# Kernel tuning notes

Hardware: AMD Instinct MI355X
Metric: run time of the kernel (lower is better)

The kernel has to match this reference:

```python
import jax, jax.numpy as jnp
import numpy as np
from jax import lax

K_RATIO = 0.5  # args['k_ratio'], eval (non-training) branch
K_SIZE = 5     # args['gaussian_smooth']['k_size']
C_SIGMA = 1.0  # args['gaussian_smooth']['c_sigma']


def _gaussian_kernel(k_size=K_SIZE, sigma=C_SIGMA):
    # matches Communication.init_gaussian_filter (note: 2*pi*sigma, not sigma^2, as in source)
    c = k_size // 2
    x, y = np.mgrid[-c:k_size - c, -c:k_size - c]
    g = 1.0 / (2.0 * np.pi * sigma) * np.exp(-(np.square(x) + np.square(y)) / (2.0 * np.square(sigma)))
    return jnp.asarray(g, jnp.float32)[None, None]  # (1,1,k,k) OIHW, bias is zero


def setup_inputs() -> dict:
    key = jax.random.key(0)
    conf = jax.random.normal(jax.random.fold_in(key, 1), (8, 6, 4, 512, 512), jnp.float32)
    warp = jnp.ones((8, 1, 512, 512), jnp.float32)
    return {"confidence_maps": conf, "warp_masks": warp, "gauss_kernel": _gaussian_kernel()}


def reference(confidence_maps, warp_masks, gauss_kernel):
    # confidence_maps: (B, L, C, H, W); warp_masks: (B, 1, H, W); gauss_kernel: (1,1,k,k)
    B, L, C, H, W = confidence_maps.shape
    # sigmoid + max over anchor dim, keepdim -> (B, L, 1, H, W)
    m = jnp.max(jax.nn.sigmoid(confidence_maps), axis=2, keepdims=True)
    m = m * warp_masks[:, None]  # broadcast warp mask over agents
    # frozen gaussian smoothing conv, SAME padding (stride 1, pad (k-1)//2)
    sm = lax.conv_general_dilated(m.reshape(B * L, 1, H, W), gauss_kernel,
                                  window_strides=(1, 1), padding='SAME',
                                  dimension_numbers=('NCHW', 'OIHW', 'NCHW'))
    flat = sm.reshape(B, L, H * W)
    K = int(H * W * K_RATIO)  # static k, eval k_ratio branch
    _, idx = lax.top_k(flat, K)  # (B, L, K)
    mask = jnp.zeros_like(flat).at[
        jnp.arange(B)[:, None, None], jnp.arange(L)[None, :, None], idx
    ].set(1.0)  # scatter ones at top-k positions
    # communication rate computed BEFORE ego mask is forced to 1 (as in source)
    rate = jnp.mean(jnp.sum(mask[:, 1:], axis=(1, 2)) / ((L - 1) * H * W))
    mask = mask.reshape(B, L, H, W).at[:, 0].set(1.0)  # ego agent keeps everything
    return mask.reshape(B * L, 1, H, W), rate
```

## Files before the change

kernel.cpp:

```cpp
#include <hip/hip_runtime.h>


#define NROWSEL 40
#define NPIX    262144
#define KSEL    131072
#define CAND_CAP 512
#define KAPPA    3
#define KSCALE   1048576.0f
#define KMAX     1048575.0f

#define OFF_KEY  0ull
#define OFF_H1   41943040ull
#define OFF_H2   42106880ull
#define OFF_ST   42270720ull
#define OFF_CC   42271040ull
#define OFF_CI   42271200ull
#define OFF_CK   42353120ull
#define META_U32 82040

__device__ __forceinline__ float m_val_f32(const float* __restrict__ confr,
                                           const float* __restrict__ warpr,
                                           int gy, int gx) {
  if (gy < 0 || gy >= 512 || gx < 0 || gx >= 512) return 0.0f;
  int off = gy * 512 + gx;
  float x0 = confr[off];
  float x1 = confr[NPIX + off];
  float x2 = confr[2 * NPIX + off];
  float x3 = confr[3 * NPIX + off];
  float mx = fmaxf(fmaxf(x0, x1), fmaxf(x2, x3));
  float s = 1.0f / (1.0f + expf(-mx));
  return s * warpr[off];
}

__device__ __forceinline__ double m_val(const float* __restrict__ confr,
                                        const float* __restrict__ warpr,
                                        int gy, int gx) {
  if (gy < 0 || gy >= 512 || gx < 0 || gx >= 512) return 0.0;
  int off = gy * 512 + gx;
  float x0 = confr[off];
  float x1 = confr[NPIX + off];
  float x2 = confr[2 * NPIX + off];
  float x3 = confr[3 * NPIX + off];
  float mx = fmaxf(fmaxf(x0, x1), fmaxf(x2, x3));
  double s = 1.0 / (1.0 + exp(-(double)mx));
  return s * (double)warpr[off];
}

__device__ __forceinline__ void scan1024(const unsigned* __restrict__ hs,
                                         unsigned* __restrict__ red,
                                         int tid, unsigned cum0,
                                         int* bsel, unsigned* above) {
  red[tid] = hs[tid * 4] + hs[tid * 4 + 1] + hs[tid * 4 + 2] + hs[tid * 4 + 3];
  __syncthreads();
  if (tid == 0) {
    unsigned cum = cum0;
    *bsel = 0; *above = cum0;
    for (int c = 255; c >= 0; --c) {
      if (cum + red[c] >= (unsigned)KSEL) {
        unsigned cc2 = cum;
        for (int k = 3; k >= 0; --k) {
          unsigned hv = hs[c * 4 + k];
          if (cc2 + hv >= (unsigned)KSEL) { *bsel = c * 4 + k; *above = cc2; break; }
          cc2 += hv;
        }
        break;
      }
      cum += red[c];
    }
  }
}

__global__ void ego_fill_kernel(float* __restrict__ out,
                                unsigned* __restrict__ meta) {
  int i = blockIdx.x * 256 + threadIdx.x;
  int b = i >> 16;
  int o4 = i & 65535;
  float4* p = (float4*)(out + (size_t)b * 6u * NPIX) + o4;
  *p = make_float4(1.f, 1.f, 1.f, 1.f);
  if (i < META_U32) meta[i] = 0u;
}

__global__ __launch_bounds__(256) void compute_kernel(
    const float* __restrict__ conf, const float* __restrict__ warp,
    const float* __restrict__ gk, unsigned* __restrict__ keys,
    unsigned* __restrict__ hist1) {
  const int blk = blockIdx.x;
  const int j = blk >> 6;
  const int tile = blk & 63;
  const int ty0 = (tile >> 3) << 6;
  const int tx0 = (tile & 7) << 6;
  const int b = j / 5;
  const int l = j % 5 + 1;
  const int rowg = b * 6 + l;
  const float* confr = conf + (size_t)rowg * 4u * NPIX;
  const float* warpr = warp + (size_t)b * NPIX;

  __shared__ float mt[68][68];
  __shared__ float ht[68][64];
  __shared__ unsigned lh[4096];
  __shared__ float wr[5], wc[5];
  const int tid = threadIdx.x;
  if (tid < 5) {
    wr[tid] = gk[10 + tid];
    wc[tid] = gk[tid * 5 + 2] / gk[12];
  }
  for (int i = tid; i < 4096; i += 256) lh[i] = 0u;

  for (int i = tid; i < 68 * 68; i += 256) {
    int hy = i / 68, hx = i - hy * 68;
    mt[hy][hx] = m_val_f32(confr, warpr, ty0 + hy - 2, tx0 + hx - 2);
  }
  __syncthreads();

  for (int i = tid; i < 68 * 64; i += 256) {
    int hy = i >> 6, x = i & 63;
    float a = mt[hy][x] * wr[0];
    a = fmaf(wr[1], mt[hy][x + 1], a);
    a = fmaf(wr[2], mt[hy][x + 2], a);
    a = fmaf(wr[3], mt[hy][x + 3], a);
    a = fmaf(wr[4], mt[hy][x + 4], a);
    ht[hy][x] = a;
  }
  __syncthreads();

  const int txl = tid & 63;
  const int tyl = tid >> 6;
  const int cpy = tid & 3;
  unsigned* keyrow = keys + (size_t)j * NPIX;
  for (int rr = 0; rr < 16; ++rr) {
    int yy = tyl + (rr << 2);
    float acc = ht[yy][txl] * wc[0];
    acc = fmaf(wc[1], ht[yy + 1][txl], acc);
    acc = fmaf(wc[2], ht[yy + 2][txl], acc);
    acc = fmaf(wc[3], ht[yy + 3][txl], acc);
    acc = fmaf(wc[4], ht[yy + 4][txl], acc);
    unsigned k = (unsigned)fminf(fmaxf(acc * KSCALE, 0.0f), KMAX);
    keyrow[(ty0 + yy) * 512 + (tx0 + txl)] = k;
    atomicAdd(&lh[(k >> 10) * 4 + cpy], 1u);
  }
  __syncthreads();
  for (int i = tid; i < 1024; i += 256) {
    unsigned s = lh[i * 4] + lh[i * 4 + 1] + lh[i * 4 + 2] + lh[i * 4 + 3];
    if (s) atomicAdd(&hist1[j * 1024 + i], s);
  }
}

__global__ __launch_bounds__(256) void hist2_kernel(
    const unsigned* __restrict__ keys, const unsigned* __restrict__ hist1,
    unsigned* __restrict__ hist2) {
  int blk = blockIdx.x;
  int j = blk >> 5, seg = blk & 31;
  __shared__ unsigned hs[1024];
  __shared__ unsigned red[256];
  __shared__ unsigned lh[4096];
  __shared__ int s_b1;
  int tid = threadIdx.x;
  for (int i = tid; i < 1024; i += 256) hs[i] = hist1[j * 1024 + i];
  for (int i = tid; i < 4096; i += 256) lh[i] = 0u;
  __syncthreads();
  int b1; unsigned A1;
  scan1024(hs, red, tid, 0u, &b1, &A1);
  if (tid == 0) s_b1 = b1;
  __syncthreads();
  unsigned ub1 = (unsigned)s_b1;
  const uint4* kp = (const uint4*)(keys + (size_t)j * NPIX + seg * 8192);
  int c = tid & 3;
#pragma unroll
  for (int it = 0; it < 8; ++it) {
    uint4 k4 = kp[tid + it * 256];
    if ((k4.x >> 10) == ub1) atomicAdd(&lh[(k4.x & 1023u) * 4 + c], 1u);
    if ((k4.y >> 10) == ub1) atomicAdd(&lh[(k4.y & 1023u) * 4 + c], 1u);
    if ((k4.z >> 10) == ub1) atomicAdd(&lh[(k4.z & 1023u) * 4 + c], 1u);
    if ((k4.w >> 10) == ub1) atomicAdd(&lh[(k4.w & 1023u) * 4 + c], 1u);
  }
  __syncthreads();
  for (int i = tid; i < 1024; i += 256) {
    unsigned s = lh[i * 4] + lh[i * 4 + 1] + lh[i * 4 + 2] + lh[i * 4 + 3];
    if (s) atomicAdd(&hist2[j * 1024 + i], s);
  }
}

__global__ __launch_bounds__(256) void mask_gather_kernel(
    const unsigned* __restrict__ keys, const unsigned* __restrict__ hist1,
    const unsigned* __restrict__ hist2, float* __restrict__ out,
    int* __restrict__ st, unsigned* __restrict__ ccount,
    int* __restrict__ cidx, unsigned* __restrict__ ckey) {
  int blk = blockIdx.x;
  int j = blk >> 5, seg = blk & 31;
  int b = j / 5, l = j % 5 + 1;
  int rowg = b * 6 + l;
  __shared__ unsigned hs[1024];
  __shared__ unsigned red[256];
  __shared__ int s_pstar;
  int tid = threadIdx.x;
  for (int i = tid; i < 1024; i += 256) hs[i] = hist1[j * 1024 + i];
  __syncthreads();
  int b1; unsigned A1;
  scan1024(hs, red, tid, 0u, &b1, &A1);
  __syncthreads();
  for (int i = tid; i < 1024; i += 256) hs[i] = hist2[j * 1024 + i];
  __syncthreads();
  int b2; unsigned A2;
  scan1024(hs, red, tid, (tid == 0) ? A1 : 0u, &b2, &A2);
  if (tid == 0) {
    s_pstar = (b1 << 10) | b2;
    if (seg == 0) { st[j * 2] = s_pstar; st[j * 2 + 1] = (int)A2; }
  }
  __syncthreads();
  int pstar = s_pstar;

  const uint4* kp = (const uint4*)(keys + (size_t)j * NPIX + seg * 8192);
  float4* o4 = (float4*)(out + (size_t)rowg * NPIX + seg * 8192);
#pragma unroll
  for (int it = 0; it < 8; ++it) {
    int q = tid + it * 256;
    uint4 k4 = kp[q];
    unsigned w[4] = {k4.x, k4.y, k4.z, k4.w};
    float4 mv;
    float* mf = (float*)&mv;
#pragma unroll
    for (int e = 0; e < 4; ++e) {
      int k = (int)w[e];
      mf[e] = k > pstar + KAPPA ? 1.f : 0.f;
      if (k >= pstar - KAPPA && k <= pstar + KAPPA) {
        unsigned s = atomicAdd(&ccount[j], 1u);
        if (s < CAND_CAP) {
          cidx[j * CAND_CAP + s] = seg * 8192 + q * 4 + e;
          ckey[j * CAND_CAP + s] = (unsigned)k;
        }
      }
    }
    o4[q] = mv;
  }
}

__global__ __launch_bounds__(256) void resolve_kernel(
    const float* __restrict__ conf, const float* __restrict__ warp,
    const float* __restrict__ gk, const int* __restrict__ st,
    const unsigned* __restrict__ ccount, const int* __restrict__ cidx,
    const unsigned* __restrict__ ckey, float* __restrict__ out) {
  int j = blockIdx.x;
  int b = j / 5, l = j % 5 + 1;
  int rowg = b * 6 + l;
  const float* confr = conf + (size_t)rowg * 4u * NPIX;
  const float* warpr = warp + (size_t)b * NPIX;
  __shared__ double vs[CAND_CAP];
  __shared__ int ids[CAND_CAP];
  __shared__ unsigned red[256];
  __shared__ double g[25];
  int tid = threadIdx.x;
  if (tid < 25) g[tid] = (double)gk[tid];
  int pstar = st[j * 2];
  int A2 = st[j * 2 + 1];
  int C = (int)min(ccount[j], (unsigned)CAND_CAP);
  __syncthreads();
  unsigned cnt = 0;
  for (int i = tid; i < C; i += 256) {
    int idx = cidx[j * CAND_CAP + i];
    cnt += (int)ckey[j * CAND_CAP + i] > pstar ? 1u : 0u;
    int y = idx >> 9, x = idx & 511;
    double acc = 0.0;
#pragma unroll
    for (int dy = 0; dy < 5; ++dy)
#pragma unroll
      for (int dx = 0; dx < 5; ++dx)
        acc = fma(g[dy * 5 + dx], m_val(confr, warpr, y + dy - 2, x + dx - 2), acc);
    vs[i] = acc;
    ids[i] = idx;
  }
  red[tid] = cnt;
  __syncthreads();
  for (int s = 128; s > 0; s >>= 1) {
    if (tid < s) red[tid] += red[tid + s];
    __syncthreads();
  }
  int R = KSEL - A2 + (int)red[0];
  for (int i = tid; i < C; i += 256) {
    double vi = vs[i];
    int ii = ids[i];
    int rank = 0;
    for (int q = 0; q < C; ++q) {
      double vq = vs[q];
      rank += (vq > vi) || (vq == vi && ids[q] < ii) ? 1 : 0;
    }
    if (rank < R) out[(size_t)rowg * NPIX + ii] = 1.0f;
  }
  if (j == 0 && tid == 0) out[12582912] = 0.5f;
}

extern "C" void kernel_launch(void* const* d_in, const int* in_sizes, int n_in,
                              void* d_out, int out_size, void* d_ws, size_t ws_size,
                              hipStream_t stream) {
  const float* conf = (const float*)d_in[0];
  const float* warp = (const float*)d_in[1];
  const float* gk   = (const float*)d_in[2];
  float* out = (float*)d_out;
  char* ws = (char*)d_ws;

  unsigned* keys = (unsigned*)(ws + OFF_KEY);
  unsigned* h1   = (unsigned*)(ws + OFF_H1);
  unsigned* h2   = (unsigned*)(ws + OFF_H2);
  int*      st   = (int*)(ws + OFF_ST);
  unsigned* cc   = (unsigned*)(ws + OFF_CC);
  int*      ci   = (int*)(ws + OFF_CI);
  unsigned* ck   = (unsigned*)(ws + OFF_CK);

  ego_fill_kernel<<<2048, 256, 0, stream>>>(out, h1);
  compute_kernel<<<NROWSEL * 64, 256, 0, stream>>>(conf, warp, gk, keys, h1);
  hist2_kernel<<<NROWSEL * 32, 256, 0, stream>>>(keys, h1, h2);
  mask_gather_kernel<<<NROWSEL * 32, 256, 0, stream>>>(keys, h1, h2, out, st, cc, ci, ck);
  resolve_kernel<<<NROWSEL, 256, 0, stream>>>(conf, warp, gk, st, cc, ci, ck, out);
}
```

Baseline: 149.7 us.

## Fuse separable blur passes in registers and rebalance radix histogram to 256/4096 bins

```diff
diff --git a/kernel.cpp b/kernel.cpp
--- a/kernel.cpp
+++ b/kernel.cpp
@@ -11,12 +11,12 @@
 
 #define OFF_KEY  0ull
 #define OFF_H1   41943040ull
-#define OFF_H2   42106880ull
-#define OFF_ST   42270720ull
-#define OFF_CC   42271040ull
-#define OFF_CI   42271200ull
-#define OFF_CK   42353120ull
-#define META_U32 82040
+#define OFF_H2   41984000ull
+#define OFF_ST   42639360ull
+#define OFF_CC   42639680ull
+#define OFF_CI   42639840ull
+#define OFF_CK   42721760ull
+#define META_U32 174200
 
 __device__ __forceinline__ float m_val_f32(const float* __restrict__ confr,
                                            const float* __restrict__ warpr,
@@ -46,11 +46,25 @@
   return s * (double)warpr[off];
 }
 
-__device__ __forceinline__ void scan1024(const unsigned* __restrict__ hs,
+__device__ __forceinline__ void scan256(const unsigned* __restrict__ cs,
+                                        unsigned cum0, int& bsel,
+                                        unsigned& above) {
+  unsigned cum = cum0;
+  bsel = 0; above = cum0;
+  for (int c = 255; c >= 0; --c) {
+    if (cum + cs[c] >= (unsigned)KSEL) { bsel = c; above = cum; break; }
+    cum += cs[c];
+  }
+}
+
+__device__ __forceinline__ void scan4096(const unsigned* __restrict__ hs,
                                          unsigned* __restrict__ red,
                                          int tid, unsigned cum0,
                                          int* bsel, unsigned* above) {
-  red[tid] = hs[tid * 4] + hs[tid * 4 + 1] + hs[tid * 4 + 2] + hs[tid * 4 + 3];
+  unsigned s = 0;
+#pragma unroll 4
+  for (int k = 0; k < 16; ++k) s += hs[tid * 16 + k];
+  red[tid] = s;
   __syncthreads();
   if (tid == 0) {
     unsigned cum = cum0;
@@ -58,9 +72,9 @@
     for (int c = 255; c >= 0; --c) {
       if (cum + red[c] >= (unsigned)KSEL) {
         unsigned cc2 = cum;
-        for (int k = 3; k >= 0; --k) {
-          unsigned hv = hs[c * 4 + k];
-          if (cc2 + hv >= (unsigned)KSEL) { *bsel = c * 4 + k; *above = cc2; break; }
+        for (int k = 15; k >= 0; --k) {
+          unsigned hv = hs[c * 16 + k];
+          if (cc2 + hv >= (unsigned)KSEL) { *bsel = c * 16 + k; *above = cc2; break; }
           cc2 += hv;
         }
         break;
@@ -96,15 +110,14 @@
   const float* warpr = warp + (size_t)b * NPIX;
 
   __shared__ float mt[68][68];
-  __shared__ float ht[68][64];
-  __shared__ unsigned lh[4096];
+  __shared__ unsigned lh[1024];
   __shared__ float wr[5], wc[5];
   const int tid = threadIdx.x;
   if (tid < 5) {
     wr[tid] = gk[10 + tid];
     wc[tid] = gk[tid * 5 + 2] / gk[12];
   }
-  for (int i = tid; i < 4096; i += 256) lh[i] = 0u;
+  for (int i = tid; i < 1024; i += 256) lh[i] = 0u;
 
   for (int i = tid; i < 68 * 68; i += 256) {
     int hy = i / 68, hx = i - hy * 68;
@@ -112,36 +125,38 @@
   }
   __syncthreads();
 
-  for (int i = tid; i < 68 * 64; i += 256) {
-    int hy = i >> 6, x = i & 63;
-    float a = mt[hy][x] * wr[0];
-    a = fmaf(wr[1], mt[hy][x + 1], a);
-    a = fmaf(wr[2], mt[hy][x + 2], a);
-    a = fmaf(wr[3], mt[hy][x + 3], a);
-    a = fmaf(wr[4], mt[hy][x + 4], a);
-    ht[hy][x] = a;
-  }
-  __syncthreads();
-
   const int txl = tid & 63;
-  const int tyl = tid >> 6;
+  const int y0 = (tid >> 6) << 4;
   const int cpy = tid & 3;
   unsigned* keyrow = keys + (size_t)j * NPIX;
-  for (int rr = 0; rr < 16; ++rr) {
-    int yy = tyl + (rr << 2);
-    float acc = ht[yy][txl] * wc[0];
-    acc = fmaf(wc[1], ht[yy + 1][txl], acc);
-    acc = fmaf(wc[2], ht[yy + 2][txl], acc);
-    acc = fmaf(wc[3], ht[yy + 3][txl], acc);
-    acc = fmaf(wc[4], ht[yy + 4][txl], acc);
+
+#define HROW(r) ({ float a_ = mt[(r)][txl] * wr[0];            \
+                   a_ = fmaf(wr[1], mt[(r)][txl + 1], a_);     \
+                   a_ = fmaf(wr[2], mt[(r)][txl + 2], a_);     \
+                   a_ = fmaf(wr[3], mt[(r)][txl + 3], a_);     \
+                   fmaf(wr[4], mt[(r)][txl + 4], a_); })
+
+  float h0 = HROW(y0);
+  float h1 = HROW(y0 + 1);
+  float h2 = HROW(y0 + 2);
+  float h3 = HROW(y0 + 3);
+  for (int yy = y0; yy < y0 + 16; ++yy) {
+    float h4 = HROW(yy + 4);
+    float acc = h0 * wc[0];
+    acc = fmaf(wc[1], h1, acc);
+    acc = fmaf(wc[2], h2, acc);
+    acc = fmaf(wc[3], h3, acc);
+    acc = fmaf(wc[4], h4, acc);
     unsigned k = (unsigned)fminf(fmaxf(acc * KSCALE, 0.0f), KMAX);
     keyrow[(ty0 + yy) * 512 + (tx0 + txl)] = k;
-    atomicAdd(&lh[(k >> 10) * 4 + cpy], 1u);
-  }
-  __syncthreads();
-  for (int i = tid; i < 1024; i += 256) {
-    unsigned s = lh[i * 4] + lh[i * 4 + 1] + lh[i * 4 + 2] + lh[i * 4 + 3];
-    if (s) atomicAdd(&hist1[j * 1024 + i], s);
+    atomicAdd(&lh[(k >> 12) * 4 + cpy], 1u);
+    h0 = h1; h1 = h2; h2 = h3; h3 = h4;
+  }
+#undef HROW
+  __syncthreads();
+  if (tid < 256) {
+    unsigned s = lh[tid * 4] + lh[tid * 4 + 1] + lh[tid * 4 + 2] + lh[tid * 4 + 3];
+    if (s) atomicAdd(&hist1[j * 256 + tid], s);
   }
 }
 
@@ -150,33 +165,34 @@
     unsigned* __restrict__ hist2) {
   int blk = blockIdx.x;
   int j = blk >> 5, seg = blk & 31;
-  __shared__ unsigned hs[1024];
-  __shared__ unsigned red[256];
-  __shared__ unsigned lh[4096];
+  __shared__ unsigned hs[256];
+  __shared__ unsigned lh[8192];
   __shared__ int s_b1;
   int tid = threadIdx.x;
-  for (int i = tid; i < 1024; i += 256) hs[i] = hist1[j * 1024 + i];
-  for (int i = tid; i < 4096; i += 256) lh[i] = 0u;
-  __syncthreads();
-  int b1; unsigned A1;
-  scan1024(hs, red, tid, 0u, &b1, &A1);
-  if (tid == 0) s_b1 = b1;
+  hs[tid] = hist1[j * 256 + tid];
+  for (int i = tid; i < 8192; i += 256) lh[i] = 0u;
+  __syncthreads();
+  if (tid == 0) {
+    int b1; unsigned A1;
+    scan256(hs, 0u, b1, A1);
+    s_b1 = b1;
+  }
   __syncthreads();
   unsigned ub1 = (unsigned)s_b1;
   const uint4* kp = (const uint4*)(keys + (size_t)j * NPIX + seg * 8192);
-  int c = tid & 3;
+  int c = tid & 1;
 #pragma unroll
   for (int it = 0; it < 8; ++it) {
     uint4 k4 = kp[tid + it * 256];
-    if ((k4.x >> 10) == ub1) atomicAdd(&lh[(k4.x & 1023u) * 4 + c], 1u);
-    if ((k4.y >> 10) == ub1) atomicAdd(&lh[(k4.y & 1023u) * 4 + c], 1u);
-    if ((k4.z >> 10) == ub1) atomicAdd(&lh[(k4.z & 1023u) * 4 + c], 1u);
-    if ((k4.w >> 10) == ub1) atomicAdd(&lh[(k4.w & 1023u) * 4 + c], 1u);
-  }
-  __syncthreads();
-  for (int i = tid; i < 1024; i += 256) {
-    unsigned s = lh[i * 4] + lh[i * 4 + 1] + lh[i * 4 + 2] + lh[i * 4 + 3];
-    if (s) atomicAdd(&hist2[j * 1024 + i], s);
+    if ((k4.x >> 12) == ub1) atomicAdd(&lh[(k4.x & 4095u) * 2 + c], 1u);
+    if ((k4.y >> 12) == ub1) atomicAdd(&lh[(k4.y & 4095u) * 2 + c], 1u);
+    if ((k4.z >> 12) == ub1) atomicAdd(&lh[(k4.z & 4095u) * 2 + c], 1u);
+    if ((k4.w >> 12) == ub1) atomicAdd(&lh[(k4.w & 4095u) * 2 + c], 1u);
+  }
+  __syncthreads();
+  for (int i = tid; i < 4096; i += 256) {
+    unsigned s = lh[i * 2] + lh[i * 2 + 1];
+    if (s) atomicAdd(&hist2[j * 4096 + i], s);
   }
 }
 
@@ -189,21 +205,21 @@
   int j = blk >> 5, seg = blk & 31;
   int b = j / 5, l = j % 5 + 1;
   int rowg = b * 6 + l;
-  __shared__ unsigned hs[1024];
+  __shared__ unsigned hs[4096];
   __shared__ unsigned red[256];
   __shared__ int s_pstar;
   int tid = threadIdx.x;
-  for (int i = tid; i < 1024; i += 256) hs[i] = hist1[j * 1024 + i];
-  __syncthreads();
-  int b1; unsigned A1;
-  scan1024(hs, red, tid, 0u, &b1, &A1);
-  __syncthreads();
-  for (int i = tid; i < 1024; i += 256) hs[i] = hist2[j * 1024 + i];
+  hs[tid] = hist1[j * 256 + tid];
+  __syncthreads();
+  int b1 = 0; unsigned A1 = 0;
+  if (tid == 0) scan256(hs, 0u, b1, A1);
+  __syncthreads();
+  for (int i = tid; i < 4096; i += 256) hs[i] = hist2[j * 4096 + i];
   __syncthreads();
   int b2; unsigned A2;
-  scan1024(hs, red, tid, (tid == 0) ? A1 : 0u, &b2, &A2);
+  scan4096(hs, red, tid, A1, &b2, &A2);
   if (tid == 0) {
-    s_pstar = (b1 << 10) | b2;
+    s_pstar = (b1 << 12) | b2;
     if (seg == 0) { st[j * 2] = s_pstar; st[j * 2 + 1] = (int)A2; }
   }
   __syncthreads();
```

Result: slower. 155.6 us (+4.0%).
